# Performance work log

Measured on AMD Instinct MI355X. Metric: run time of the kernel, lower is better.

The kernel has to match this reference:

```python
import jax, jax.numpy as jnp
import numpy as np

K = 32          # num_cones
D = 512         # decoder feature dim (feature_mapper in_features)
VOX = 32 * 32 * 32
N = 524288      # query points
EPS = 1e-8

CONE_ADDER = jnp.array([-0.8, -0.8, -0.8, 0.05, 0.1, -1.0, -1.0, -1.0], jnp.float32)
CONE_MULT = jnp.array([1.0, 1.0, 1.0, 0.01, 0.03, 1.7, 1.7, 1.7], jnp.float32)


def setup_inputs() -> dict:
    key = jax.random.key(0)
    ks = jax.random.split(key, 8)
    return {
        "voxel_data": jax.random.normal(ks[0], (1, VOX), jnp.float32),
        "query_points": jax.random.uniform(ks[1], (N, 3), jnp.float32, minval=-1.0, maxval=1.0),
        "initial_centers": jax.random.normal(ks[2], (K, 3), jnp.float32) * 0.3,
        # learned params (encoder MLP -> 512, decoder MLP 512->512, feature_mapper 512->K*8)
        "W_enc": jax.random.normal(ks[3], (VOX, D), jnp.float32) * 0.01,
        "b_enc": jnp.zeros((D,), jnp.float32),
        "W_dec": jax.random.normal(ks[4], (D, D), jnp.float32) * 0.04,
        "b_dec": jnp.zeros((D,), jnp.float32),
        "W_map": jax.random.normal(ks[5], (D, K * 8), jnp.float32) * 0.04,
        "b_map": jnp.zeros((K * 8,), jnp.float32),
    }


def determine_cone_sdf(q, p):
    # q: [N,3] query points; p: [K,8] = center(3), radius, height, orientation(3)
    centers = p[:, 0:3]            # [K,3]
    radii = p[:, 3]                # [K]
    heights = p[:, 4]              # [K]
    orient = p[:, 5:8]             # [K,3]
    axis = orient / (jnp.linalg.norm(orient, axis=-1, keepdims=True) + EPS)  # [K,3]
    v = q[:, None, :] - centers[None, :, :]                # [N,K,3]
    proj = jnp.einsum("nkd,kd->nk", v, axis)               # signed dist along axis [N,K]
    perp = jnp.linalg.norm(v - proj[..., None] * axis[None, :, :], axis=-1)  # [N,K]
    # lateral (slanted) surface: radius tapers linearly from base (proj=0) to apex (proj=height)
    slant = perp - radii[None, :] * (1.0 - proj / (heights[None, :] + EPS))
    cap = jnp.abs(proj) - heights[None, :]                 # end caps
    return jnp.maximum(slant, cap)                         # [N,K]


def reference(voxel_data, query_points, initial_centers,
              W_enc, b_enc, W_dec, b_dec, W_map, b_map):
    # encoder (global feature) -> decoder -> feature_mapper
    feat = jax.nn.relu(voxel_data @ W_enc + b_enc)     # [1, D]
    dec = jax.nn.relu(feat @ W_dec + b_dec)            # [1, D]
    cone_params = (dec @ W_map + b_map).reshape(K, 8)  # [K, 8]
    # sigmoid + affine rescale into valid geometric ranges
    cone_params = jax.nn.sigmoid(cone_params) * CONE_MULT + CONE_ADDER
    cone_sdf = determine_cone_sdf(query_points, cone_params)  # [N, K]
    return cone_sdf, cone_params
```

## Files before the change

### kernel.cpp

```cpp
#include <hip/hip_runtime.h>
#include <math.h>

#define DD 512
#define KC 32
#define NQ 524288
#define EPSF 1e-8f
#define CONE_STRIDE 13

typedef float f4 __attribute__((ext_vector_type(4)));

__device__ __constant__ float c_mult[8]  = {1.f, 1.f, 1.f, 0.01f, 0.03f, 1.7f, 1.7f, 1.7f};
__device__ __constant__ float c_adder[8] = {-0.8f, -0.8f, -0.8f, 0.05f, 0.1f, -1.f, -1.f, -1.f};

__global__ __launch_bounds__(512) void k_enc(const float* __restrict__ vox,
                                             const float* __restrict__ Wenc,
                                             const float* __restrict__ Wdec,
                                             const float* __restrict__ Wmap,
                                             float* __restrict__ partialT) {
    __shared__ float4 red4[512];
    const int t = threadIdx.x;
    const int b = blockIdx.x;
    f4 pf = {0.f, 0.f, 0.f, 0.f};
    const int idx = b * 512 + t;
    if (idx < 65536 + 32768) {
        pf = (idx < 65536) ? reinterpret_cast<const f4*>(Wdec)[idx]
                           : reinterpret_cast<const f4*>(Wmap)[idx - 65536];
    }
    const int g  = t >> 7;
    const int c4 = (t & 127) << 2;
    const int v0 = b * 64;
    float4 acc = make_float4(0.f, 0.f, 0.f, 0.f);
    #pragma unroll
    for (int it = 0; it < 16; ++it) {
        const int v = v0 + it * 4 + g;
        const float sv = vox[v];
        const float4 w = *reinterpret_cast<const float4*>(&Wenc[(size_t)v * DD + c4]);
        acc.x += sv * w.x; acc.y += sv * w.y; acc.z += sv * w.z; acc.w += sv * w.w;
    }
    red4[t] = acc;
    __syncthreads();
    const float* red = reinterpret_cast<const float*>(red4);
    const float s = red[t] + red[512 + t] + red[1024 + t] + red[1536 + t];
    partialT[(size_t)b * 512 + t] = s;
    asm volatile("" :: "v"(pf.x), "v"(pf.y));
}

__global__ __launch_bounds__(512) void k_dec(const float* __restrict__ partialT,
                                             const float* __restrict__ benc,
                                             const float* __restrict__ Wdec,
                                             float* __restrict__ decPart) {
    __shared__ float4 red4[512];
    __shared__ float wsum[8];
    const int t = threadIdx.x;
    const int g = t >> 7;
    const int j = t & 127;
    const int i = blockIdx.x * 4 + g;
    float s = 0.f;
    #pragma unroll
    for (int m = 0; m < 4; ++m)
        s += partialT[(size_t)(j + 128 * m) * 512 + i];
    #pragma unroll
    for (int off = 32; off >= 1; off >>= 1) s += __shfl_xor(s, off, 64);
    if ((t & 63) == 0) wsum[t >> 6] = s;
    __syncthreads();
    float fi = wsum[2 * g] + wsum[2 * g + 1] + benc[i];
    fi = fi > 0.f ? fi : 0.f;
    const float4 w = *reinterpret_cast<const float4*>(&Wdec[(size_t)i * DD + (j << 2)]);
    red4[t] = make_float4(fi * w.x, fi * w.y, fi * w.z, fi * w.w);
    __syncthreads();
    const float* red = reinterpret_cast<const float*>(red4);
    const float s2 = red[t] + red[512 + t] + red[1024 + t] + red[1536 + t];
    decPart[(size_t)blockIdx.x * 512 + t] = s2;
}

__global__ __launch_bounds__(512) void k_cones(const float* __restrict__ decPart,
                                               const float* __restrict__ bdec,
                                               const float* __restrict__ Wmap,
                                               const float* __restrict__ bmap,
                                               const float* __restrict__ q,
                                               float* __restrict__ out_params,
                                               float* __restrict__ cones,
                                               float* __restrict__ qsink) {
    const int t = threadIdx.x;
    const int b = blockIdx.x;
    if (b >= 8) {
        const f4* q4 = reinterpret_cast<const f4*>(q);
        f4 acc = {0.f, 0.f, 0.f, 0.f};
        const int nth = 248 * 512;
        for (int i = (b - 8) * 512 + t; i < (NQ * 3) / 4; i += nth) {
            f4 v = q4[i];
            acc.x += v.x; acc.y += v.y; acc.z += v.z; acc.w += v.w;
        }
        if (t == 0) qsink[b] = acc.x + acc.y + acc.z + acc.w;
        return;
    }
    __shared__ f4 red[512];
    __shared__ float dec_lds[DD];
    __shared__ float psum[512];
    __shared__ float pbuf[32];
    {
        const f4* dP4 = reinterpret_cast<const f4*>(decPart);
        const int d4 = t & 127;
        const int bc = t >> 7;
        f4 a = {0.f, 0.f, 0.f, 0.f};
        #pragma unroll
        for (int m = 0; m < 32; ++m) {
            const f4 v = dP4[(size_t)(bc * 32 + m) * 128 + d4];
            a.x += v.x; a.y += v.y; a.z += v.z; a.w += v.w;
        }
        red[t] = a;
        __syncthreads();
        if (t < 128) {
            f4 s = red[t];
            const f4 s1 = red[t + 128], s2 = red[t + 256], s3 = red[t + 384];
            s.x += s1.x + s2.x + s3.x; s.y += s1.y + s2.y + s3.y;
            s.z += s1.z + s2.z + s3.z; s.w += s1.w + s2.w + s3.w;
            const f4 bd = reinterpret_cast<const f4*>(bdec)[t];
            dec_lds[4*t+0] = fmaxf(s.x + bd.x, 0.f);
            dec_lds[4*t+1] = fmaxf(s.y + bd.y, 0.f);
            dec_lds[4*t+2] = fmaxf(s.z + bd.z, 0.f);
            dec_lds[4*t+3] = fmaxf(s.w + bd.w, 0.f);
        }
        __syncthreads();
    }
    {
        const int jj = t & 31;
        const int c  = t >> 5;
        const int j  = b * 32 + jj;
        float acc = 0.f;
        #pragma unroll
        for (int r = 0; r < 32; ++r) {
            const int i = c * 32 + r;
            acc += dec_lds[i] * Wmap[(size_t)i * 256 + j];
        }
        psum[c * 32 + jj] = acc;
        __syncthreads();
        if (t < 32) {
            float m = 0.f;
            #pragma unroll
            for (int cc = 0; cc < 16; ++cc) m += psum[cc * 32 + t];
            const float tot = m + bmap[b * 32 + t];
            const float sig = 1.f / (1.f + expf(-tot));
            const float val = sig * c_mult[t & 7] + c_adder[t & 7];
            out_params[b * 32 + t] = val;
            pbuf[t] = val;
        }
        __syncthreads();
    }
    if (t < 4) {
        const float* p = &pbuf[t * 8];
        const float cx = p[0], cy = p[1], cz = p[2];
        const float r  = p[3], hh = p[4];
        const float ox = p[5], oy = p[6], oz = p[7];
        const float nrm = sqrtf(ox*ox + oy*oy + oz*oz) + EPSF;
        const float inv = 1.f / nrm;
        const float inv_h = 1.f / (hh + EPSF);
        float* ck = &cones[(b * 4 + t) * CONE_STRIDE];
        ck[0] = cx;        ck[1] = cy;       ck[2] = cz;
        ck[3] = ox * inv;  ck[4] = oy * inv; ck[5] = oz * inv;
        ck[6] = r;         ck[7] = hh;       ck[8] = inv_h;
        ck[9] = r * inv_h; ck[10] = 0.f;     ck[11] = 0.f;  ck[12] = 0.f;
    }
}

__global__ __launch_bounds__(256) void k_sdf(const float* __restrict__ q,
                                             const float* __restrict__ cones,
                                             float* __restrict__ out) {
    __shared__ float c[KC * CONE_STRIDE];
    const int t = threadIdx.x;
    c[t] = cones[t];
    if (t < KC * CONE_STRIDE - 256) c[256 + t] = cones[256 + t];
    __syncthreads();
    const int k0 = (t & 7) << 2;
    float cx[4], cy[4], cz[4], ax[4], ay[4], az[4], cr[4], chh[4], rih[4];
    #pragma unroll
    for (int kk = 0; kk < 4; ++kk) {
        const float* ck = &c[(k0 + kk) * CONE_STRIDE];
        cx[kk] = ck[0]; cy[kk] = ck[1]; cz[kk] = ck[2];
        ax[kk] = ck[3]; ay[kk] = ck[4]; az[kk] = ck[5];
        cr[kk] = ck[6]; chh[kk] = ck[7]; rih[kk] = ck[9];
    }
    const size_t qbase = (size_t)blockIdx.x * 256;
    const int nl = t >> 3;
    #pragma unroll
    for (int tile = 0; tile < 8; ++tile) {
        const size_t n = qbase + tile * 32 + nl;
        const float qx = q[n * 3 + 0];
        const float qy = q[n * 3 + 1];
        const float qz = q[n * 3 + 2];
        f4 o;
        #pragma unroll
        for (int kk = 0; kk < 4; ++kk) {
            const float vx = qx - cx[kk];
            const float vy = qy - cy[kk];
            const float vz = qz - cz[kk];
            const float proj = vx*ax[kk] + vy*ay[kk] + vz*az[kk];
            const float d2 = vx*vx + vy*vy + vz*vz;
            float pp = d2 - proj * proj;
            pp = pp > 0.f ? pp : 0.f;
            const float perp = sqrtf(pp);
            const float slant = perp - cr[kk] + rih[kk] * proj;
            const float cap = fabsf(proj) - chh[kk];
            o[kk] = slant > cap ? slant : cap;
        }
        __builtin_nontemporal_store(o, reinterpret_cast<f4*>(&out[n * (size_t)KC + k0]));
    }
}

extern "C" void kernel_launch(void* const* d_in, const int* in_sizes, int n_in,
                              void* d_out, int out_size, void* d_ws, size_t ws_size,
                              hipStream_t stream) {
    const float* vox  = (const float*)d_in[0];
    const float* q    = (const float*)d_in[1];
    const float* Wenc = (const float*)d_in[3];
    const float* benc = (const float*)d_in[4];
    const float* Wdec = (const float*)d_in[5];
    const float* bdec = (const float*)d_in[6];
    const float* Wmap = (const float*)d_in[7];
    const float* bmap = (const float*)d_in[8];
    float* out = (float*)d_out;
    float* ws  = (float*)d_ws;

    float* partialT = ws;
    float *decPart, *cones, *qsink;
    const size_t fullF = 262144 + 65536 + 512 + 256;
    if (ws_size >= fullF * sizeof(float)) {
        decPart = ws + 262144;
        cones   = decPart + 65536;
        qsink   = cones + 512;
    } else {
        decPart = out;
        cones   = ws + 262144;
        qsink   = cones + 512;
    }
    float* out_params = out + (size_t)NQ * KC;

    k_enc<<<512, 512, 0, stream>>>(vox, Wenc, Wdec, Wmap, partialT);
    k_dec<<<128, 512, 0, stream>>>(partialT, benc, Wdec, decPart);
    k_cones<<<256, 512, 0, stream>>>(decPart, bdec, Wmap, bmap, q,
                                     out_params, cones, qsink);
    k_sdf<<<2048, 256, 0, stream>>>(q, cones, out);
}
```

Baseline: 45.39 us.

## Merge decoder and cone-param kernels into one small kernel, move query prefetch into encoder

Removes the separate k_dec launch. The encoder partials are now reduced, the decoder matvec is run and the cone params are computed all inside one 8-block k_mid kernel, where each block redundantly repeats the full 512x512 decoder matvec. The L2 warm-up read of the query points moves from k_cones into k_enc. This saves a launch and the decPart round trip, but the work in k_mid runs on only 8 blocks with long serial loops, so that kernel may take longer per block.

```diff
diff --git a/kernel.cpp b/kernel.cpp
--- a/kernel.cpp
+++ b/kernel.cpp
@@ -16,15 +16,22 @@
                                              const float* __restrict__ Wenc,
                                              const float* __restrict__ Wdec,
                                              const float* __restrict__ Wmap,
+                                             const float* __restrict__ q,
                                              float* __restrict__ partialT) {
     __shared__ float4 red4[512];
     const int t = threadIdx.x;
     const int b = blockIdx.x;
+    const int idx = b * 512 + t;
     f4 pf = {0.f, 0.f, 0.f, 0.f};
-    const int idx = b * 512 + t;
     if (idx < 65536 + 32768) {
         pf = (idx < 65536) ? reinterpret_cast<const f4*>(Wdec)[idx]
                            : reinterpret_cast<const f4*>(Wmap)[idx - 65536];
+    }
+    const f4* q4 = reinterpret_cast<const f4*>(q);
+    f4 qp = {0.f, 0.f, 0.f, 0.f};
+    for (int i = idx; i < (NQ * 3) / 4; i += 262144) {
+        const f4 v = q4[i];
+        qp.x += v.x; qp.y += v.y; qp.z += v.z; qp.w += v.w;
     }
     const int g  = t >> 7;
     const int c4 = (t & 127) << 2;
@@ -42,70 +49,32 @@
     const float* red = reinterpret_cast<const float*>(red4);
     const float s = red[t] + red[512 + t] + red[1024 + t] + red[1536 + t];
     partialT[(size_t)b * 512 + t] = s;
-    asm volatile("" :: "v"(pf.x), "v"(pf.y));
-}
-
-__global__ __launch_bounds__(512) void k_dec(const float* __restrict__ partialT,
+    asm volatile("" :: "v"(pf.x), "v"(qp.x));
+}
+
+__global__ __launch_bounds__(512) void k_mid(const float* __restrict__ partialT,
                                              const float* __restrict__ benc,
                                              const float* __restrict__ Wdec,
-                                             float* __restrict__ decPart) {
-    __shared__ float4 red4[512];
-    __shared__ float wsum[8];
-    const int t = threadIdx.x;
-    const int g = t >> 7;
-    const int j = t & 127;
-    const int i = blockIdx.x * 4 + g;
-    float s = 0.f;
-    #pragma unroll
-    for (int m = 0; m < 4; ++m)
-        s += partialT[(size_t)(j + 128 * m) * 512 + i];
-    #pragma unroll
-    for (int off = 32; off >= 1; off >>= 1) s += __shfl_xor(s, off, 64);
-    if ((t & 63) == 0) wsum[t >> 6] = s;
-    __syncthreads();
-    float fi = wsum[2 * g] + wsum[2 * g + 1] + benc[i];
-    fi = fi > 0.f ? fi : 0.f;
-    const float4 w = *reinterpret_cast<const float4*>(&Wdec[(size_t)i * DD + (j << 2)]);
-    red4[t] = make_float4(fi * w.x, fi * w.y, fi * w.z, fi * w.w);
-    __syncthreads();
-    const float* red = reinterpret_cast<const float*>(red4);
-    const float s2 = red[t] + red[512 + t] + red[1024 + t] + red[1536 + t];
-    decPart[(size_t)blockIdx.x * 512 + t] = s2;
-}
-
-__global__ __launch_bounds__(512) void k_cones(const float* __restrict__ decPart,
-                                               const float* __restrict__ bdec,
-                                               const float* __restrict__ Wmap,
-                                               const float* __restrict__ bmap,
-                                               const float* __restrict__ q,
-                                               float* __restrict__ out_params,
-                                               float* __restrict__ cones,
-                                               float* __restrict__ qsink) {
-    const int t = threadIdx.x;
-    const int b = blockIdx.x;
-    if (b >= 8) {
-        const f4* q4 = reinterpret_cast<const f4*>(q);
-        f4 acc = {0.f, 0.f, 0.f, 0.f};
-        const int nth = 248 * 512;
-        for (int i = (b - 8) * 512 + t; i < (NQ * 3) / 4; i += nth) {
-            f4 v = q4[i];
-            acc.x += v.x; acc.y += v.y; acc.z += v.z; acc.w += v.w;
-        }
-        if (t == 0) qsink[b] = acc.x + acc.y + acc.z + acc.w;
-        return;
-    }
+                                             const float* __restrict__ bdec,
+                                             const float* __restrict__ Wmap,
+                                             const float* __restrict__ bmap,
+                                             float* __restrict__ out_params,
+                                             float* __restrict__ cones) {
     __shared__ f4 red[512];
+    __shared__ float feat_lds[DD];
     __shared__ float dec_lds[DD];
     __shared__ float psum[512];
     __shared__ float pbuf[32];
+    const int t = threadIdx.x;
+    const int b = blockIdx.x;
     {
-        const f4* dP4 = reinterpret_cast<const f4*>(decPart);
+        const f4* pT4 = reinterpret_cast<const f4*>(partialT);
         const int d4 = t & 127;
         const int bc = t >> 7;
         f4 a = {0.f, 0.f, 0.f, 0.f};
-        #pragma unroll
-        for (int m = 0; m < 32; ++m) {
-            const f4 v = dP4[(size_t)(bc * 32 + m) * 128 + d4];
+        #pragma unroll 8
+        for (int m = 0; m < 128; ++m) {
+            const f4 v = pT4[(size_t)(bc * 128 + m) * 128 + d4];
             a.x += v.x; a.y += v.y; a.z += v.z; a.w += v.w;
         }
         red[t] = a;
@@ -115,12 +84,20 @@
             const f4 s1 = red[t + 128], s2 = red[t + 256], s3 = red[t + 384];
             s.x += s1.x + s2.x + s3.x; s.y += s1.y + s2.y + s3.y;
             s.z += s1.z + s2.z + s3.z; s.w += s1.w + s2.w + s3.w;
-            const f4 bd = reinterpret_cast<const f4*>(bdec)[t];
-            dec_lds[4*t+0] = fmaxf(s.x + bd.x, 0.f);
-            dec_lds[4*t+1] = fmaxf(s.y + bd.y, 0.f);
-            dec_lds[4*t+2] = fmaxf(s.z + bd.z, 0.f);
-            dec_lds[4*t+3] = fmaxf(s.w + bd.w, 0.f);
-        }
+            const f4 be = reinterpret_cast<const f4*>(benc)[t];
+            feat_lds[4*t+0] = fmaxf(s.x + be.x, 0.f);
+            feat_lds[4*t+1] = fmaxf(s.y + be.y, 0.f);
+            feat_lds[4*t+2] = fmaxf(s.z + be.z, 0.f);
+            feat_lds[4*t+3] = fmaxf(s.w + be.w, 0.f);
+        }
+        __syncthreads();
+    }
+    {
+        float acc = 0.f;
+        #pragma unroll 8
+        for (int i = 0; i < DD; ++i)
+            acc += feat_lds[i] * Wdec[(size_t)i * DD + t];
+        dec_lds[t] = fmaxf(acc + bdec[t], 0.f);
         __syncthreads();
     }
     {
@@ -221,23 +198,19 @@
     float* out = (float*)d_out;
     float* ws  = (float*)d_ws;
 
-    float* partialT = ws;
-    float *decPart, *cones, *qsink;
-    const size_t fullF = 262144 + 65536 + 512 + 256;
-    if (ws_size >= fullF * sizeof(float)) {
-        decPart = ws + 262144;
-        cones   = decPart + 65536;
-        qsink   = cones + 512;
+    float *partialT, *cones;
+    const size_t needF = 262144 + 512;
+    if (ws_size >= needF * sizeof(float)) {
+        partialT = ws;
+        cones    = ws + 262144;
     } else {
-        decPart = out;
-        cones   = ws + 262144;
-        qsink   = cones + 512;
+        partialT = out;
+        cones    = ws;
     }
     float* out_params = out + (size_t)NQ * KC;
 
-    k_enc<<<512, 512, 0, stream>>>(vox, Wenc, Wdec, Wmap, partialT);
-    k_dec<<<128, 512, 0, stream>>>(partialT, benc, Wdec, decPart);
-    k_cones<<<256, 512, 0, stream>>>(decPart, bdec, Wmap, bmap, q,
-                                     out_params, cones, qsink);
+    k_enc<<<512, 512, 0, stream>>>(vox, Wenc, Wdec, Wmap, q, partialT);
+    k_mid<<<8, 512, 0, stream>>>(partialT, benc, Wdec, bdec, Wmap, bmap,
+                                 out_params, cones);
     k_sdf<<<2048, 256, 0, stream>>>(q, cones, out);
 }
```

After: 72.22 us. 59.1% more time.
